# Kernel optimization log

Hardware: AMD Instinct MI355X
Metric: run time of the kernel (lower is better)

The kernel has to match this reference:

```python
import jax, jax.numpy as jnp
import numpy as np

HEADS = 8
DIM_HEAD = 64
MAX_FREQ = 10.0


def _rope_tables(n):
    # RotaryEmbedding(dim_head//2): inv_freq over arange(0, 32, 2)/32 -> 16 freqs
    half = DIM_HEAD // 2  # 32
    inv_freq = 1.0 / (MAX_FREQ ** (jnp.arange(0, half, 2, dtype=jnp.float32) / half))  # [16]
    t = jnp.arange(n, dtype=jnp.float32)
    freqs = t[:, None] * inv_freq[None, :]          # [n, 16]
    freqs = jnp.concatenate([freqs, freqs], axis=-1)  # [n, 32]
    return jnp.cos(freqs), jnp.sin(freqs)


def _apply_rope(x, cos, sin):
    # x: [b, h, n, 64] split into pairs (d=32, r=2)
    b, h, n, dh = x.shape
    xr = x.reshape(b, h, n, dh // 2, 2)
    x1, x2 = xr[..., 0], xr[..., 1]                 # [b, h, n, 32]
    o1 = x1 * cos - x2 * sin                        # cos/sin: [n, 32] broadcast
    o2 = x1 * sin + x2 * cos
    return jnp.stack([o1, o2], axis=-1).reshape(b, h, n, dh)


def setup_inputs() -> dict:
    key = jax.random.key(0)
    k1, k2, k3, k4, k5, k6 = jax.random.split(key, 6)
    b, n, d = 2, 4096, 512
    inner = HEADS * DIM_HEAD  # 512
    s = lambda fan_in: 1.0 / np.sqrt(fan_in)
    return {
        "x": jax.random.normal(k1, (b, n, d), dtype=jnp.float32),
        "w_qkv": jax.random.normal(k2, (d, 3 * inner), dtype=jnp.float32) * s(d),
        "w_gates": jax.random.normal(k3, (d, HEADS), dtype=jnp.float32) * s(d),
        "b_gates": jax.random.normal(k4, (HEADS,), dtype=jnp.float32) * s(d),
        "w_out": jax.random.normal(k5, (inner, d), dtype=jnp.float32) * s(inner),
        "b_out": jax.random.normal(k6, (d,), dtype=jnp.float32) * s(inner),
    }


def reference(x, w_qkv, w_gates, b_gates, w_out, b_out):
    b, n, d = x.shape
    h, dh = HEADS, DIM_HEAD
    scale = dh ** -0.5

    qkv = x @ w_qkv                                  # [b, n, 3*h*dh]
    q, k, v = jnp.split(qkv, 3, axis=-1)
    to_bhnd = lambda t: t.reshape(b, n, h, dh).transpose(0, 2, 1, 3)
    q, k, v = to_bhnd(q), to_bhnd(k), to_bhnd(v)

    cos, sin = _rope_tables(n)
    q = _apply_rope(q, cos, sin)
    k = _apply_rope(k, cos, sin)

    dots = jnp.einsum('bhid,bhjd->bhij', q, k) * scale   # [b, h, n, n]
    attn = jax.nn.softmax(dots, axis=-1)

    gates = jax.nn.sigmoid(x @ w_gates + b_gates)        # [b, n, h]
    out = jnp.einsum('bhij,bhjd->bhid', attn, v)         # [b, h, n, dh]
    out = out * gates.transpose(0, 2, 1)[..., None]      # per-head sigmoid gate
    out = out.transpose(0, 2, 1, 3).reshape(b, n, h * dh)
    return out @ w_out + b_out
```

## Files before the change

kernel.cpp:

```cpp
#include <hip/hip_runtime.h>

typedef unsigned short u16;
typedef unsigned int u32;
typedef __attribute__((ext_vector_type(2))) unsigned int u32x2;
typedef __attribute__((ext_vector_type(4))) float f32x4;
typedef __attribute__((ext_vector_type(16))) float f32x16;
typedef __attribute__((ext_vector_type(8))) short s16x8;
typedef __attribute__((ext_vector_type(4))) short s16x4;

union U64 { u32 d[2]; s16x4 v; };
union U128 { u32 d[4]; s16x8 v; };

__device__ __forceinline__ u16 f2bf(float f) {
  u32 u = __builtin_bit_cast(u32, f);
  u += 0x7fffu + ((u >> 16) & 1u);
  return (u16)(u >> 16);
}

__device__ __forceinline__ u32 cvt_pk(float a, float b) {
  u32 r;
  asm("v_cvt_pk_bf16_f32 %0, %1, %2" : "=v"(r) : "v"(a), "v"(b));
  return r;
}

__device__ __forceinline__ void gload16(const void* g, void* l) {
  __builtin_amdgcn_global_load_lds((const __attribute__((address_space(1))) void*)g,
                                   (__attribute__((address_space(3))) void*)l, 16, 0, 0);
}

__global__ void rope_tab_kernel(float* __restrict__ ct, float* __restrict__ st) {
  int idx = blockIdx.x * 256 + threadIdx.x;
  int row = idx >> 5, col = idx & 31;
  int j = col & 15;
  float invf = __powf(10.0f, -(float)j * (1.0f / 16.0f));
  float ang = (float)row * invf;
  ct[idx] = cosf(ang);
  st[idx] = sinf(ang);
}

__global__ void convert_x_kernel(const float* __restrict__ x, u16* __restrict__ xb) {
  int i = blockIdx.x * 256 + threadIdx.x;
  f32x4 a = ((const f32x4*)x)[i * 2 + 0];
  f32x4 b = ((const f32x4*)x)[i * 2 + 1];
  s16x8 o;
  o[0] = (short)f2bf(a[0]); o[1] = (short)f2bf(a[1]);
  o[2] = (short)f2bf(a[2]); o[3] = (short)f2bf(a[3]);
  o[4] = (short)f2bf(b[0]); o[5] = (short)f2bf(b[1]);
  o[6] = (short)f2bf(b[2]); o[7] = (short)f2bf(b[3]);
  ((s16x8*)xb)[i] = o;
}

__global__ void transpose_conv_kernel(const float* __restrict__ in, u16* __restrict__ out,
                                      int R, int C) {
  __shared__ float tl[32][33];
  int c0 = blockIdx.x * 32, r0 = blockIdx.y * 32;
  int tx = threadIdx.x, ty = threadIdx.y;
#pragma unroll
  for (int i = 0; i < 4; i++)
    tl[ty + i * 8][tx] = in[(size_t)(r0 + ty + i * 8) * C + c0 + tx];
  __syncthreads();
#pragma unroll
  for (int i = 0; i < 4; i++)
    out[(size_t)(c0 + ty + i * 8) * R + r0 + tx] = f2bf(tl[tx][ty + i * 8]);
}

__global__ void gates_kernel(const float* __restrict__ x, const float* __restrict__ wg,
                             const float* __restrict__ bg, float* __restrict__ gates) {
  int t = threadIdx.x;
  int lane = t & 63, w = t >> 6;
  int row = blockIdx.x * 4 + w;
  float acc[8] = {0, 0, 0, 0, 0, 0, 0, 0};
#pragma unroll
  for (int kk = 0; kk < 8; kk++) {
    int k = kk * 64 + lane;
    float xv = x[(size_t)row * 512 + k];
    f32x4 w0 = ((const f32x4*)(wg + (size_t)k * 8))[0];
    f32x4 w1 = ((const f32x4*)(wg + (size_t)k * 8))[1];
    acc[0] += xv * w0[0]; acc[1] += xv * w0[1]; acc[2] += xv * w0[2]; acc[3] += xv * w0[3];
    acc[4] += xv * w1[0]; acc[5] += xv * w1[1]; acc[6] += xv * w1[2]; acc[7] += xv * w1[3];
  }
#pragma unroll
  for (int off = 32; off >= 1; off >>= 1) {
#pragma unroll
    for (int h = 0; h < 8; h++) acc[h] += __shfl_xor(acc[h], off);
  }
  if (lane < 8) {
    float v = acc[0];
#pragma unroll
    for (int hh = 1; hh < 8; hh++) if (lane == hh) v = acc[hh];
    v += bg[lane];
    gates[(size_t)row * 8 + lane] = 1.0f / (1.0f + __expf(-v));
  }
}

template <int EPI>
__global__ __launch_bounds__(256, 2) void gemm_kernel(
    const u16* __restrict__ A, const u16* __restrict__ Bt, float* __restrict__ outp, int Nc,
    const float* __restrict__ cost, const float* __restrict__ sint,
    const float* __restrict__ bias, u16* __restrict__ qkv, u16* __restrict__ vws) {
  __shared__ u16 Al[128][72];
  __shared__ u16 Bl[128][72];
  int t = threadIdx.x;
  int nb = Nc >> 7;
  int bm = blockIdx.x / nb, bn = blockIdx.x % nb;
  int m0 = bm << 7, n0 = bn << 7;
  int w = t >> 6, lane = t & 63, c = lane & 15, g = lane >> 4;
  int wr = w >> 1, wc = w & 1;
  f32x4 acc[4][4] = {};
  int ldr = t >> 3, ldj = t & 7;
  const u16* Ag = A + (size_t)m0 * 512;
  const u16* Bg = Bt + (size_t)n0 * 512;
  for (int k0 = 0; k0 < 512; k0 += 64) {
    __syncthreads();
#pragma unroll
    for (int rr = 0; rr < 4; rr++) {
      int row = ldr + rr * 32;
      *(s16x8*)&Al[row][ldj * 8] = *(const s16x8*)(Ag + (size_t)row * 512 + k0 + ldj * 8);
      *(s16x8*)&Bl[row][ldj * 8] = *(const s16x8*)(Bg + (size_t)row * 512 + k0 + ldj * 8);
    }
    __syncthreads();
#pragma unroll
    for (int ks = 0; ks < 2; ks++) {
      s16x8 af[4], bf[4];
#pragma unroll
      for (int mt = 0; mt < 4; mt++)
        af[mt] = *(const s16x8*)&Al[wr * 64 + mt * 16 + c][ks * 32 + g * 8];
#pragma unroll
      for (int nt = 0; nt < 4; nt++)
        bf[nt] = *(const s16x8*)&Bl[wc * 64 + nt * 16 + c][ks * 32 + g * 8];
#pragma unroll
      for (int mt = 0; mt < 4; mt++)
#pragma unroll
        for (int nt = 0; nt < 4; nt++)
          acc[mt][nt] = __builtin_amdgcn_mfma_f32_16x16x32_bf16(af[mt], bf[nt], acc[mt][nt], 0, 0, 0);
    }
  }
  if (EPI == 0) {
    int sect = n0 >> 9;
    if (sect < 2) {
#pragma unroll
      for (int mt = 0; mt < 4; mt++) {
#pragma unroll
      for (int nt = 0; nt < 4; nt++) {
#pragma unroll
          for (int r = 0; r < 4; r++) {
            int mrow = m0 + wr * 64 + mt * 16 + g * 4 + r;
            int cg = n0 + wc * 64 + nt * 16 + c;
            float val = acc[mt][nt][r];
            float other = __shfl_xor(val, 1);
            int p = (cg & 63) >> 1;
            int nidx = mrow & 4095;
            float cv = cost[nidx * 32 + p];
            float sv = sint[nidx * 32 + p];
            float o = (cg & 1) ? (other * sv + val * cv) : (val * cv - other * sv);
            if (sect == 0) o *= 0.18033688011f;
            qkv[(size_t)mrow * 1536 + cg] = f2bf(o);
          }
        }
      }
    } else {
#pragma unroll
      for (int mt = 0; mt < 4; mt++) {
#pragma unroll
        for (int nt = 0; nt < 4; nt++) {
          int cg = n0 + wc * 64 + nt * 16 + c;
          int vcol = cg - 1024;
          int hh = vcol >> 6, dh = vcol & 63;
          int mrowb = m0 + wr * 64 + mt * 16 + g * 4;
          int bb = mrowb >> 12, nn = mrowb & 4095;
          U64 u;
          u.d[0] = cvt_pk(acc[mt][nt][0], acc[mt][nt][1]);
          u.d[1] = cvt_pk(acc[mt][nt][2], acc[mt][nt][3]);
          *(s16x4*)(vws + ((size_t)(bb * 8 + hh) * 64 + dh) * 4096 + nn) = u.v;
        }
      }
    }
  } else {
#pragma unroll
    for (int mt = 0; mt < 4; mt++) {
#pragma unroll
      for (int nt = 0; nt < 4; nt++) {
#pragma unroll
        for (int r = 0; r < 4; r++) {
          int mrow = m0 + wr * 64 + mt * 16 + g * 4 + r;
          int cg = n0 + wc * 64 + nt * 16 + c;
          outp[(size_t)mrow * 512 + cg] = acc[mt][nt][r] + bias[cg];
        }
      }
    }
  }
}

__global__ __launch_bounds__(256, 2) void attn_kernel(const u16* __restrict__ qkv,
                                                      const u16* __restrict__ vT,
                                                      const float* __restrict__ gates,
                                                      u16* __restrict__ ao) {
  __shared__ u16 Kl[2][4096];
  __shared__ u16 Vl[2][4096];
  int t = threadIdx.x;
  int bh = blockIdx.x >> 5, qblk = blockIdx.x & 31;
  int b = bh >> 3, h = bh & 7;
  int w = t >> 6, lane = t & 63;
  int c32 = lane & 31, hi = lane >> 5;
  int q0 = qblk * 128 + w * 32;

  const char* qb = (const char*)qkv;
  const char* vb = (const char*)vT;
  u32 D0 = (u32)(w * 2048 + lane * 16);
  u32 D1 = D0 + 1024;
  u32 u0 = D0 ^ (((D0 >> 7) & 7) << 4);
  u32 u1 = D1 ^ (((D1 >> 7) & 7) << 4);
  const char* ksrc0 = qb + ((size_t)(b * 4096 + (D0 >> 7)) * 1536 + 512 + h * 64) * 2 + (u0 & 127);
  const char* ksrc1 = qb + ((size_t)(b * 4096 + (D1 >> 7)) * 1536 + 512 + h * 64) * 2 + (u1 & 127);
  const char* vsrc0 = vb + ((size_t)((b * 8 + h) * 64 + (D0 >> 7)) * 4096) * 2 + (u0 & 127);
  const char* vsrc1 = vb + ((size_t)((b * 8 + h) * 64 + (D1 >> 7)) * 4096) * 2 + (u1 & 127);

  s16x8 qf[4];
  {
    const u16* qp = qkv + (size_t)(b * 4096 + q0 + c32) * 1536 + h * 64 + hi * 8;
#pragma unroll
    for (int ks = 0; ks < 4; ks++) qf[ks] = *(const s16x8*)(qp + ks * 16);
  }

  s16x8 ones;
#pragma unroll
  for (int i = 0; i < 8; i++) ones[i] = (short)0x3f80;

  u32 rsw = (u32)((c32 & 7) << 4);
  const char* klb = (const char*)&Kl[0][0] + c32 * 128;
  const char* vlb = (const char*)&Vl[0][0] + c32 * 128;

  f32x16 acco[2] = {};
  f32x16 accl = {};

  {
    char* kd = (char*)&Kl[0][0] + w * 2048;
    char* vd = (char*)&Vl[0][0] + w * 2048;
    gload16(ksrc0, kd);
    gload16(ksrc1, kd + 1024);
    gload16(vsrc0, vd);
    gload16(vsrc1, vd + 1024);
  }
  __syncthreads();

  int cur = 0;
  for (int tile = 0; tile < 64; ++tile) {
    if (tile < 63) {
      int nbuf = cur ^ 1;
      size_t ka = (size_t)(tile + 1) * 196608;
      size_t va = (size_t)(tile + 1) * 128;
      char* kd = (char*)&Kl[0][0] + nbuf * 8192 + w * 2048;
      char* vd = (char*)&Vl[0][0] + nbuf * 8192 + w * 2048;
      gload16(ksrc0 + ka, kd);
      gload16(ksrc1 + ka, kd + 1024);
      gload16(vsrc0 + va, vd);
      gload16(vsrc1 + va, vd + 1024);
    }

    const char* kl = klb + cur * 8192;
    f32x16 sc[2] = {};
    __builtin_amdgcn_s_setprio(1);
#pragma unroll
    for (int kb = 0; kb < 2; kb++) {
#pragma unroll
      for (int ks = 0; ks < 4; ks++) {
        s16x8 kf = *(const s16x8*)(kl + kb * 4096 + (((u32)(ks * 32 + hi * 16)) ^ rsw));
        sc[kb] = __builtin_amdgcn_mfma_f32_32x32x16_bf16(kf, qf[ks], sc[kb], 0, 0, 0);
      }
    }
    __builtin_amdgcn_s_setprio(0);

#pragma unroll
    for (int kb = 0; kb < 2; kb++)
#pragma unroll
      for (int r = 0; r < 16; r++) sc[kb][r] = exp2f(sc[kb][r]);

    U128 pf[4];
#pragma unroll
    for (int kb = 0; kb < 2; kb++) {
#pragma unroll
      for (int s = 0; s < 2; s++) {
        u32 a1 = cvt_pk(sc[kb][s * 8 + 0], sc[kb][s * 8 + 1]);
        u32 b1 = cvt_pk(sc[kb][s * 8 + 4], sc[kb][s * 8 + 5]);
        u32 a2 = cvt_pk(sc[kb][s * 8 + 2], sc[kb][s * 8 + 3]);
        u32 b2 = cvt_pk(sc[kb][s * 8 + 6], sc[kb][s * 8 + 7]);
        u32x2 r1 = __builtin_amdgcn_permlane32_swap(a1, b1, false, false);
        u32x2 r2 = __builtin_amdgcn_permlane32_swap(a2, b2, false, false);
        pf[kb * 2 + s].d[0] = r1[0];
        pf[kb * 2 + s].d[1] = r2[0];
        pf[kb * 2 + s].d[2] = r1[1];
        pf[kb * 2 + s].d[3] = r2[1];
      }
    }

    const char* vl = vlb + cur * 8192;
    __builtin_amdgcn_s_setprio(1);
#pragma unroll
    for (int ks = 0; ks < 4; ks++) {
#pragma unroll
      for (int db = 0; db < 2; db++) {
        s16x8 vf = *(const s16x8*)(vl + db * 4096 + (((u32)(ks * 32 + hi * 16)) ^ rsw));
        acco[db] = __builtin_amdgcn_mfma_f32_32x32x16_bf16(vf, pf[ks].v, acco[db], 0, 0, 0);
      }
      accl = __builtin_amdgcn_mfma_f32_32x32x16_bf16(ones, pf[ks].v, accl, 0, 0, 0);
    }
    __builtin_amdgcn_s_setprio(0);

    __syncthreads();
    cur ^= 1;
  }

  float linv = 1.0f / accl[0];
  int row = b * 4096 + q0 + c32;
  float gr = gates[(size_t)row * 8 + h] * linv;
  u16* op = ao + (size_t)row * 512 + h * 64 + hi * 4;
#pragma unroll
  for (int db = 0; db < 2; db++)
#pragma unroll
    for (int grp = 0; grp < 4; grp++) {
      U64 u;
      u.d[0] = cvt_pk(acco[db][grp * 4 + 0] * gr, acco[db][grp * 4 + 1] * gr);
      u.d[1] = cvt_pk(acco[db][grp * 4 + 2] * gr, acco[db][grp * 4 + 3] * gr);
      *(s16x4*)(op + db * 32 + grp * 8) = u.v;
    }
}

extern "C" void kernel_launch(void* const* d_in, const int* in_sizes, int n_in,
                              void* d_out, int out_size, void* d_ws, size_t ws_size,
                              hipStream_t stream) {
  (void)in_sizes; (void)n_in; (void)out_size; (void)ws_size;
  const float* x = (const float*)d_in[0];
  const float* w_qkv = (const float*)d_in[1];
  const float* w_gates = (const float*)d_in[2];
  const float* b_gates = (const float*)d_in[3];
  const float* w_out = (const float*)d_in[4];
  const float* b_out = (const float*)d_in[5];
  float* out = (float*)d_out;

  char* ws = (char*)d_ws;
  size_t off = 0;
  u16* qkv_ws = (u16*)(ws + off); off += (size_t)2 * 4096 * 1536 * 2;
  u16* vws    = (u16*)(ws + off); off += (size_t)2 * 8 * 64 * 4096 * 2;
  u16* x_bf   = (u16*)(ws + off); off += (size_t)8192 * 512 * 2;
  u16* wqkvT  = (u16*)(ws + off); off += (size_t)1536 * 512 * 2;
  u16* woutT  = (u16*)(ws + off); off += (size_t)512 * 512 * 2;
  float* cost = (float*)(ws + off); off += (size_t)4096 * 32 * 4;
  float* sint = (float*)(ws + off); off += (size_t)4096 * 32 * 4;
  float* gts  = (float*)(ws + off); off += (size_t)8192 * 8 * 4;
  u16* attno  = (u16*)(ws + off); off += (size_t)8192 * 512 * 2;

  hipLaunchKernelGGL(rope_tab_kernel, dim3(512), dim3(256), 0, stream, cost, sint);
  hipLaunchKernelGGL(convert_x_kernel, dim3(2048), dim3(256), 0, stream, x, x_bf);
  hipLaunchKernelGGL(transpose_conv_kernel, dim3(48, 16), dim3(32, 8), 0, stream,
                     w_qkv, wqkvT, 512, 1536);
  hipLaunchKernelGGL(transpose_conv_kernel, dim3(16, 16), dim3(32, 8), 0, stream,
                     w_out, woutT, 512, 512);
  hipLaunchKernelGGL(gates_kernel, dim3(2048), dim3(256), 0, stream, x, w_gates, b_gates, gts);
  hipLaunchKernelGGL(gemm_kernel<0>, dim3((8192 / 128) * (1536 / 128)), dim3(256), 0, stream,
                     x_bf, wqkvT, nullptr, 1536, cost, sint, nullptr, qkv_ws, vws);
  hipLaunchKernelGGL(attn_kernel, dim3(512), dim3(256), 0, stream, qkv_ws, vws, gts, attno);
  hipLaunchKernelGGL(gemm_kernel<1>, dim3((8192 / 128) * (512 / 128)), dim3(256), 0, stream,
                     attno, woutT, out, 512, nullptr, nullptr, b_out, nullptr, nullptr);
}
```

Baseline: 261.6 us.

## Split the KV sequence across two wave groups per attention block and combine through LDS

```diff
diff --git a/kernel.cpp b/kernel.cpp
--- a/kernel.cpp
+++ b/kernel.cpp
@@ -141,7 +141,7 @@
 #pragma unroll
       for (int mt = 0; mt < 4; mt++) {
 #pragma unroll
-      for (int nt = 0; nt < 4; nt++) {
+        for (int nt = 0; nt < 4; nt++) {
 #pragma unroll
           for (int r = 0; r < 4; r++) {
             int mrow = m0 + wr * 64 + mt * 16 + g * 4 + r;
@@ -191,29 +191,30 @@
   }
 }
 
-__global__ __launch_bounds__(256, 2) void attn_kernel(const u16* __restrict__ qkv,
+__global__ __launch_bounds__(512, 4) void attn_kernel(const u16* __restrict__ qkv,
                                                       const u16* __restrict__ vT,
                                                       const float* __restrict__ gates,
                                                       u16* __restrict__ ao) {
-  __shared__ u16 Kl[2][4096];
-  __shared__ u16 Vl[2][4096];
+  __shared__ char smem[65536];
   int t = threadIdx.x;
   int bh = blockIdx.x >> 5, qblk = blockIdx.x & 31;
   int b = bh >> 3, h = bh & 7;
   int w = t >> 6, lane = t & 63;
+  int s = w >> 2, ws = w & 3;
   int c32 = lane & 31, hi = lane >> 5;
-  int q0 = qblk * 128 + w * 32;
+  int q0 = qblk * 128 + ws * 32;
+  int kvbase = s * 2048;
 
   const char* qb = (const char*)qkv;
-  const char* vb = (const char*)vT;
-  u32 D0 = (u32)(w * 2048 + lane * 16);
+  const char* vbp = (const char*)vT;
+  u32 D0 = (u32)(ws * 2048 + lane * 16);
   u32 D1 = D0 + 1024;
   u32 u0 = D0 ^ (((D0 >> 7) & 7) << 4);
   u32 u1 = D1 ^ (((D1 >> 7) & 7) << 4);
-  const char* ksrc0 = qb + ((size_t)(b * 4096 + (D0 >> 7)) * 1536 + 512 + h * 64) * 2 + (u0 & 127);
-  const char* ksrc1 = qb + ((size_t)(b * 4096 + (D1 >> 7)) * 1536 + 512 + h * 64) * 2 + (u1 & 127);
-  const char* vsrc0 = vb + ((size_t)((b * 8 + h) * 64 + (D0 >> 7)) * 4096) * 2 + (u0 & 127);
-  const char* vsrc1 = vb + ((size_t)((b * 8 + h) * 64 + (D1 >> 7)) * 4096) * 2 + (u1 & 127);
+  const char* ksrc0 = qb + ((size_t)(b * 4096 + kvbase + (D0 >> 7)) * 1536 + 512 + h * 64) * 2 + (u0 & 127);
+  const char* ksrc1 = qb + ((size_t)(b * 4096 + kvbase + (D1 >> 7)) * 1536 + 512 + h * 64) * 2 + (u1 & 127);
+  const char* vsrc0 = vbp + ((size_t)((b * 8 + h) * 64 + (D0 >> 7)) * 4096 + kvbase) * 2 + (u0 & 127);
+  const char* vsrc1 = vbp + ((size_t)((b * 8 + h) * 64 + (D1 >> 7)) * 4096 + kvbase) * 2 + (u1 & 127);
 
   s16x8 qf[4];
   {
@@ -227,30 +228,28 @@
   for (int i = 0; i < 8; i++) ones[i] = (short)0x3f80;
 
   u32 rsw = (u32)((c32 & 7) << 4);
-  const char* klb = (const char*)&Kl[0][0] + c32 * 128;
-  const char* vlb = (const char*)&Vl[0][0] + c32 * 128;
+  char* kset = smem + s * 16384;
+  char* vset = smem + 32768 + s * 16384;
+  const char* klb = kset + c32 * 128;
+  const char* vlb = vset + c32 * 128;
 
   f32x16 acco[2] = {};
   f32x16 accl = {};
 
-  {
-    char* kd = (char*)&Kl[0][0] + w * 2048;
-    char* vd = (char*)&Vl[0][0] + w * 2048;
-    gload16(ksrc0, kd);
-    gload16(ksrc1, kd + 1024);
-    gload16(vsrc0, vd);
-    gload16(vsrc1, vd + 1024);
-  }
+  gload16(ksrc0, kset + ws * 2048);
+  gload16(ksrc1, kset + ws * 2048 + 1024);
+  gload16(vsrc0, vset + ws * 2048);
+  gload16(vsrc1, vset + ws * 2048 + 1024);
   __syncthreads();
 
   int cur = 0;
-  for (int tile = 0; tile < 64; ++tile) {
-    if (tile < 63) {
+  for (int tile = 0; tile < 32; ++tile) {
+    if (tile < 31) {
       int nbuf = cur ^ 1;
       size_t ka = (size_t)(tile + 1) * 196608;
       size_t va = (size_t)(tile + 1) * 128;
-      char* kd = (char*)&Kl[0][0] + nbuf * 8192 + w * 2048;
-      char* vd = (char*)&Vl[0][0] + nbuf * 8192 + w * 2048;
+      char* kd = kset + nbuf * 8192 + ws * 2048;
+      char* vd = vset + nbuf * 8192 + ws * 2048;
       gload16(ksrc0 + ka, kd);
       gload16(ksrc1 + ka, kd + 1024);
       gload16(vsrc0 + va, vd);
@@ -279,17 +278,17 @@
 #pragma unroll
     for (int kb = 0; kb < 2; kb++) {
 #pragma unroll
-      for (int s = 0; s < 2; s++) {
-        u32 a1 = cvt_pk(sc[kb][s * 8 + 0], sc[kb][s * 8 + 1]);
-        u32 b1 = cvt_pk(sc[kb][s * 8 + 4], sc[kb][s * 8 + 5]);
-        u32 a2 = cvt_pk(sc[kb][s * 8 + 2], sc[kb][s * 8 + 3]);
-        u32 b2 = cvt_pk(sc[kb][s * 8 + 6], sc[kb][s * 8 + 7]);
+      for (int ss = 0; ss < 2; ss++) {
+        u32 a1 = cvt_pk(sc[kb][ss * 8 + 0], sc[kb][ss * 8 + 1]);
+        u32 b1 = cvt_pk(sc[kb][ss * 8 + 4], sc[kb][ss * 8 + 5]);
+        u32 a2 = cvt_pk(sc[kb][ss * 8 + 2], sc[kb][ss * 8 + 3]);
+        u32 b2 = cvt_pk(sc[kb][ss * 8 + 6], sc[kb][ss * 8 + 7]);
         u32x2 r1 = __builtin_amdgcn_permlane32_swap(a1, b1, false, false);
         u32x2 r2 = __builtin_amdgcn_permlane32_swap(a2, b2, false, false);
-        pf[kb * 2 + s].d[0] = r1[0];
-        pf[kb * 2 + s].d[1] = r2[0];
-        pf[kb * 2 + s].d[2] = r1[1];
-        pf[kb * 2 + s].d[3] = r2[1];
+        pf[kb * 2 + ss].d[0] = r1[0];
+        pf[kb * 2 + ss].d[1] = r2[0];
+        pf[kb * 2 + ss].d[2] = r1[1];
+        pf[kb * 2 + ss].d[3] = r2[1];
       }
     }
 
@@ -310,19 +309,47 @@
     cur ^= 1;
   }
 
-  float linv = 1.0f / accl[0];
-  int row = b * 4096 + q0 + c32;
-  float gr = gates[(size_t)row * 8 + h] * linv;
-  u16* op = ao + (size_t)row * 512 + h * 64 + hi * 4;
-#pragma unroll
-  for (int db = 0; db < 2; db++)
-#pragma unroll
-    for (int grp = 0; grp < 4; grp++) {
+  float* pb = (float*)smem + (size_t)(ws * 32 + c32) * 68;
+  float* lb = (float*)(smem + 36864);
+  if (s == 1) {
+#pragma unroll
+    for (int db = 0; db < 2; db++)
+#pragma unroll
+      for (int grp = 0; grp < 4; grp++) {
+        f32x4 v;
+        v[0] = acco[db][grp * 4 + 0]; v[1] = acco[db][grp * 4 + 1];
+        v[2] = acco[db][grp * 4 + 2]; v[3] = acco[db][grp * 4 + 3];
+        *(f32x4*)(pb + db * 32 + grp * 8 + hi * 4) = v;
+      }
+    if (hi == 0) lb[ws * 32 + c32] = accl[0];
+  }
+  __syncthreads();
+  if (s == 0) {
+    float linv = 1.0f / (accl[0] + lb[ws * 32 + c32]);
+    int row = b * 4096 + q0 + c32;
+    float gr = gates[(size_t)row * 8 + h] * linv;
+    u16* op = ao + (size_t)row * 512 + h * 64 + hi * 4;
+#pragma unroll
+    for (int db = 0; db < 2; db++) {
+      f32x4 v0 = *(const f32x4*)(pb + db * 32 + 0 * 8 + hi * 4);
+      f32x4 v1 = *(const f32x4*)(pb + db * 32 + 1 * 8 + hi * 4);
+      f32x4 v2 = *(const f32x4*)(pb + db * 32 + 2 * 8 + hi * 4);
+      f32x4 v3 = *(const f32x4*)(pb + db * 32 + 3 * 8 + hi * 4);
       U64 u;
-      u.d[0] = cvt_pk(acco[db][grp * 4 + 0] * gr, acco[db][grp * 4 + 1] * gr);
-      u.d[1] = cvt_pk(acco[db][grp * 4 + 2] * gr, acco[db][grp * 4 + 3] * gr);
-      *(s16x4*)(op + db * 32 + grp * 8) = u.v;
-    }
+      u.d[0] = cvt_pk((acco[db][0] + v0[0]) * gr, (acco[db][1] + v0[1]) * gr);
+      u.d[1] = cvt_pk((acco[db][2] + v0[2]) * gr, (acco[db][3] + v0[3]) * gr);
+      *(s16x4*)(op + db * 32 + 0 * 8) = u.v;
+      u.d[0] = cvt_pk((acco[db][4] + v1[0]) * gr, (acco[db][5] + v1[1]) * gr);
+      u.d[1] = cvt_pk((acco[db][6] + v1[2]) * gr, (acco[db][7] + v1[3]) * gr);
+      *(s16x4*)(op + db * 32 + 1 * 8) = u.v;
+      u.d[0] = cvt_pk((acco[db][8] + v2[0]) * gr, (acco[db][9] + v2[1]) * gr);
+      u.d[1] = cvt_pk((acco[db][10] + v2[2]) * gr, (acco[db][11] + v2[3]) * gr);
+      *(s16x4*)(op + db * 32 + 2 * 8) = u.v;
+      u.d[0] = cvt_pk((acco[db][12] + v3[0]) * gr, (acco[db][13] + v3[1]) * gr);
+      u.d[1] = cvt_pk((acco[db][14] + v3[2]) * gr, (acco[db][15] + v3[3]) * gr);
+      *(s16x4*)(op + db * 32 + 3 * 8) = u.v;
+    }
+  }
 }
 
 extern "C" void kernel_launch(void* const* d_in, const int* in_sizes, int n_in,
@@ -358,7 +385,7 @@
   hipLaunchKernelGGL(gates_kernel, dim3(2048), dim3(256), 0, stream, x, w_gates, b_gates, gts);
   hipLaunchKernelGGL(gemm_kernel<0>, dim3((8192 / 128) * (1536 / 128)), dim3(256), 0, stream,
                      x_bf, wqkvT, nullptr, 1536, cost, sint, nullptr, qkv_ws, vws);
-  hipLaunchKernelGGL(attn_kernel, dim3(512), dim3(256), 0, stream, qkv_ws, vws, gts, attno);
+  hipLaunchKernelGGL(attn_kernel, dim3(512), dim3(512), 0, stream, qkv_ws, vws, gts, attno);
   hipLaunchKernelGGL(gemm_kernel<1>, dim3((8192 / 128) * (512 / 128)), dim3(256), 0, stream,
                      attno, woutT, out, 512, nullptr, nullptr, b_out, nullptr, nullptr);
 }
```

Measured after the change: 269.5 us. 3.0% more time.
